# Performance work log

Hardware: AMD Instinct MI355X
Metric: run time of the kernel (lower is better)

The kernel has to match this reference:

```python
import jax, jax.numpy as jnp
import numpy as np

B, T, J, D_IN = 16, 128, 75, 3
HID, OUT, E = 64, 256, 300


def setup_inputs() -> dict:
    key = jax.random.key(0)
    ks = jax.random.split(key, 6)
    x = jax.random.normal(ks[0], (B, T, J, D_IN), dtype=jnp.float32)
    edge_index = jax.random.randint(ks[1], (2, E), 0, J, dtype=jnp.int64)
    W1 = jax.random.normal(ks[2], (D_IN, HID), dtype=jnp.float32) * (1.0 / np.sqrt(D_IN))
    b1 = jax.random.normal(ks[3], (HID,), dtype=jnp.float32) * 0.02
    W2 = jax.random.normal(ks[4], (HID, OUT), dtype=jnp.float32) * (1.0 / np.sqrt(HID))
    b2 = jax.random.normal(ks[5], (OUT,), dtype=jnp.float32) * 0.02
    return {"x": x, "edge_index": edge_index, "W1": W1, "b1": b1, "W2": W2, "b2": b2}


def _gcn_norm(edge_index, num_nodes, dtype):
    # PyG gcn_norm: add self-loops, norm = deg^{-1/2}[src] * deg^{-1/2}[dst]
    loops = jnp.arange(num_nodes, dtype=edge_index.dtype)
    src = jnp.concatenate([edge_index[0], loops])
    dst = jnp.concatenate([edge_index[1], loops])
    deg = jnp.zeros((num_nodes,), dtype).at[dst].add(jnp.ones_like(dst, dtype))
    dis = jax.lax.rsqrt(deg)  # deg >= 1 due to self loops
    norm = dis[src] * dis[dst]  # (E+J,)
    return src, dst, norm


def _gcn_layer(h, W, b, src, dst, norm):
    # h: (BT, J, Din) -> (BT, J, Dout). Linear first, then normalized scatter-add.
    h = h @ W
    msgs = h[:, src, :] * norm[None, :, None]        # (BT, E+J, Dout)
    agg = jnp.zeros_like(h).at[:, dst, :].add(msgs)  # (BT, J, Dout)
    return agg + b


def reference(x, edge_index, W1, b1, W2, b2):
    Bx, Tx, Jx, Dx = x.shape
    h = x.reshape(Bx * Tx, Jx, Dx)
    src, dst, norm = _gcn_norm(edge_index, Jx, x.dtype)
    h = jax.nn.gelu(_gcn_layer(h, W1, b1, src, dst, norm), approximate=False)
    h = jax.nn.gelu(_gcn_layer(h, W2, b2, src, dst, norm), approximate=False)
    return h.reshape(Bx, Tx, Jx, -1)
```

## Files before the change

### kernel.cpp

```cpp
#include <hip/hip_runtime.h>
#include <hip/hip_bf16.h>
#include <math.h>

#define J 75
#define EDGES 300
#define MAXE (EDGES + J)
#define HID 64
#define OUTF 256
#define BT 2048
#define MROWS 80
#define CSP 152

typedef __attribute__((ext_vector_type(8))) short short8;
typedef __attribute__((ext_vector_type(4))) float f32x4;

__device__ __forceinline__ unsigned short f32_to_bf16_rn(float f) {
    unsigned u = __float_as_uint(f);
    unsigned r = u + 0x7FFFu + ((u >> 16) & 1u);
    return (unsigned short)(r >> 16);
}
__device__ __forceinline__ float bf16_to_f32(unsigned short h) {
    return __uint_as_float(((unsigned)h) << 16);
}

__device__ __forceinline__ float gelu_fast(float v) {
    float u = 0.70710678118654752f * v;
    float a = fabsf(u);
    float t = __builtin_amdgcn_rcpf(fmaf(0.3275911f, a, 1.0f));
    float p = t * fmaf(t, fmaf(t, fmaf(t, fmaf(t, 1.061405429f, -1.453152027f),
                                       1.421413741f), -0.284496736f), 0.254829592f);
    float e = __expf(-a * a);
    float erfa = fmaf(-p, e, 1.0f);
    float erfu = copysignf(erfa, u);
    return 0.5f * v * (1.0f + erfu);
}

__global__ void prep_kernel(const int* __restrict__ ei,
                            const float* __restrict__ W2,
                            int* __restrict__ csr_off,
                            unsigned short* __restrict__ csr_src,
                            float* __restrict__ csr_norm,
                            unsigned short* __restrict__ Whi,
                            unsigned short* __restrict__ Wlo) {
    __shared__ int   deg[J];
    __shared__ int   off[J + 1];
    __shared__ int   cur[J];
    __shared__ float dis[J];
    const int tid = threadIdx.x;

    if (blockIdx.x < 64) {
        int t = blockIdx.x * 256 + tid;
        int j    = t & 7;
        int lane = (t >> 3) & 63;
        int nt   = (t >> 9) & 15;
        int kc   = t >> 13;
        int k = kc * 32 + (lane >> 4) * 8 + j;
        int n = nt * 16 + (lane & 15);
        float w = W2[k * OUTF + n];
        unsigned short hi = f32_to_bf16_rn(w);
        float lo = w - bf16_to_f32(hi);
        Whi[t] = hi;
        Wlo[t] = f32_to_bf16_rn(lo);
        return;
    }

    if (tid < J) { deg[tid] = 1; cur[tid] = 0; }
    __syncthreads();
    for (int e = tid; e < EDGES; e += 256)
        atomicAdd(&deg[ei[EDGES + e]], 1);
    __syncthreads();
    if (tid == 0) {
        int s = 0;
        for (int j = 0; j < J; ++j) { off[j] = s; s += deg[j]; }
        off[J] = s;
    }
    if (tid < J) dis[tid] = rsqrtf((float)deg[tid]);
    __syncthreads();
    for (int e = tid; e < EDGES; e += 256) {
        int s = ei[e], d = ei[EDGES + e];
        int p = off[d] + atomicAdd(&cur[d], 1);
        csr_src[p]  = (unsigned short)s;
        csr_norm[p] = dis[s] * dis[d];
    }
    for (int j = tid; j < J; j += 256) {
        int p = off[j] + atomicAdd(&cur[j], 1);
        csr_src[p]  = (unsigned short)j;
        csr_norm[p] = dis[j] * dis[j];
    }
    __syncthreads();
    for (int j = tid; j <= J; j += 256) csr_off[j] = off[j];
}

__global__ void __launch_bounds__(256, 3) gcn_fused_kernel(
        const float* __restrict__ xg,
        const float* __restrict__ W1,
        const float* __restrict__ b1,
        const float* __restrict__ b2,
        const int*   __restrict__ csr_off,
        const unsigned short* __restrict__ csr_src,
        const float* __restrict__ csr_norm,
        const unsigned short* __restrict__ Whi,
        const unsigned short* __restrict__ Wlo,
        float* __restrict__ outg) {
    __shared__ float xs[J * 3];
    __shared__ float ax[J * 3];
    __shared__ float Bs[J * HID];
    __shared__ __align__(16) unsigned short Csp[MROWS * CSP];
    __shared__ float W1s[3 * HID];
    __shared__ float b1s[HID];
    __shared__ float b2s[OUTF];
    __shared__ int   offs[J + 1];
    __shared__ unsigned short srcs[MAXE];
    __shared__ float nrms[MAXE];

    const int tid  = threadIdx.x;
    const int bt   = blockIdx.x;
    const int wv   = tid >> 6;
    const int lane = tid & 63;
    const int quad = lane >> 4;
    const int l16  = lane & 15;

    if (tid < J + 1) offs[tid] = csr_off[tid];
    for (int i = tid; i < MAXE; i += 256) { srcs[i] = csr_src[i]; nrms[i] = csr_norm[i]; }
    if (tid < 3 * HID) W1s[tid] = W1[tid];
    if (tid < HID)     b1s[tid] = b1[tid];
    if (tid < OUTF)    b2s[tid] = b2[tid];
    for (int i = tid; i < J * 3; i += 256)
        xs[i] = xg[bt * (J * 3) + i];
    __syncthreads();

    for (int idx = tid; idx < J * 3; idx += 256) {
        int j = idx / 3, d = idx - j * 3;
        float s = 0.f;
        int p0 = offs[j], p1 = offs[j + 1];
        for (int p = p0; p < p1; ++p) s += nrms[p] * xs[srcs[p] * 3 + d];
        ax[idx] = s;
    }
    __syncthreads();

    for (int idx = tid; idx < J * HID; idx += 256) {
        int j = idx >> 6, f = idx & 63;
        float v = ax[j * 3 + 0] * W1s[0 * HID + f]
                + ax[j * 3 + 1] * W1s[1 * HID + f]
                + ax[j * 3 + 2] * W1s[2 * HID + f]
                + b1s[f];
        Bs[idx] = gelu_fast(v);
    }
    __syncthreads();

    for (int idx = tid; idx < J * HID; idx += 256) {
        int j = idx >> 6, f = idx & 63;
        float s = 0.f, s2 = 0.f;
        int p0 = offs[j], p1 = offs[j + 1];
        int p = p0;
        for (; p + 1 < p1; p += 2) {
            int a = srcs[p], b = srcs[p + 1];
            float na = nrms[p], nb = nrms[p + 1];
            s  += na * Bs[a * HID + f];
            s2 += nb * Bs[b * HID + f];
        }
        if (p < p1) s += nrms[p] * Bs[srcs[p] * HID + f];
        s += s2;
        unsigned short hi = f32_to_bf16_rn(s);
        unsigned short lo = f32_to_bf16_rn(s - bf16_to_f32(hi));
        Csp[j * CSP + f]      = hi;
        Csp[j * CSP + 64 + f] = lo;
    }
    for (int idx = tid; idx < (MROWS - J) * 128; idx += 256) {
        int j = J + (idx >> 7), c = idx & 127;
        Csp[j * CSP + c] = 0;
    }
    __syncthreads();

    f32x4 acc[5][4];
#pragma unroll
    for (int n4 = 0; n4 < 4; ++n4) {
        float bv = b2s[wv * 64 + n4 * 16 + l16];
#pragma unroll
        for (int mt = 0; mt < 5; ++mt)
            acc[mt][n4] = (f32x4){bv, bv, bv, bv};
    }

    const short8* Whi8 = (const short8*)Whi;
    const short8* Wlo8 = (const short8*)Wlo;
#pragma unroll
    for (int kc = 0; kc < 2; ++kc) {
        short8 bhi[4], blo[4];
#pragma unroll
        for (int n4 = 0; n4 < 4; ++n4) {
            int nt = wv * 4 + n4;
            int fi = (kc * 16 + nt) * 64 + lane;
            bhi[n4] = Whi8[fi];
            blo[n4] = Wlo8[fi];
        }
#pragma unroll
        for (int mt = 0; mt < 5; ++mt) {
            const unsigned short* ar = &Csp[(mt * 16 + l16) * CSP + kc * 32 + quad * 8];
            short8 ahi = *(const short8*)ar;
            short8 alo = *(const short8*)(ar + 64);
#pragma unroll
            for (int n4 = 0; n4 < 4; ++n4) {
                acc[mt][n4] = __builtin_amdgcn_mfma_f32_16x16x32_bf16(ahi, bhi[n4], acc[mt][n4], 0, 0, 0);
                acc[mt][n4] = __builtin_amdgcn_mfma_f32_16x16x32_bf16(ahi, blo[n4], acc[mt][n4], 0, 0, 0);
                acc[mt][n4] = __builtin_amdgcn_mfma_f32_16x16x32_bf16(alo, bhi[n4], acc[mt][n4], 0, 0, 0);
            }
        }
    }

    float* outb = outg + (size_t)bt * (J * OUTF);
#pragma unroll
    for (int mt = 0; mt < 5; ++mt) {
#pragma unroll
        for (int n4 = 0; n4 < 4; ++n4) {
            int o = wv * 64 + n4 * 16 + l16;
#pragma unroll
            for (int r = 0; r < 4; ++r) {
                int row = mt * 16 + quad * 4 + r;
                if (row < J)
                    outb[row * OUTF + o] = gelu_fast(acc[mt][n4][r]);
            }
        }
    }
}

extern "C" void kernel_launch(void* const* d_in, const int* in_sizes, int n_in,
                              void* d_out, int out_size, void* d_ws, size_t ws_size,
                              hipStream_t stream) {
    const float* x  = (const float*)d_in[0];
    const int*   ei = (const int*)d_in[1];
    const float* W1 = (const float*)d_in[2];
    const float* b1 = (const float*)d_in[3];
    const float* W2 = (const float*)d_in[4];
    const float* b2 = (const float*)d_in[5];
    float* out = (float*)d_out;

    char* ws = (char*)d_ws;
    int*            csr_off  = (int*)ws;
    unsigned short* csr_src  = (unsigned short*)(ws + 512);
    float*          csr_norm = (float*)(ws + 2048);
    unsigned short* Whi      = (unsigned short*)(ws + 4096);
    unsigned short* Wlo      = (unsigned short*)(ws + 4096 + 32768);

    prep_kernel<<<65, 256, 0, stream>>>(ei, W2, csr_off, csr_src, csr_norm, Whi, Wlo);
    gcn_fused_kernel<<<BT, 256, 0, stream>>>(x, W1, b1, b2,
                                             csr_off, csr_src, csr_norm,
                                             Whi, Wlo, out);
}
```

Measured before the change: 221.3 us.

## Aggregate layer-2 via dense adjacency MFMA, tanh GELU, and higher occupancy

Precomputes a dense normalized adjacency matrix split into bf16 hi/lo fragments and performs the layer-2 neighbour aggregation as an MFMA matmul instead of a CSR gather loop. The W2 GEMM is split into two passes over output tiles to halve accumulator registers, and the launch bound rises to 4 blocks per CU with smaller LDS use. GELU is replaced by the tanh approximation, which is cheaper but deviates from the exact erf GELU in the reference.

```diff
diff --git a/kernel.cpp b/kernel.cpp
--- a/kernel.cpp
+++ b/kernel.cpp
@@ -8,8 +8,9 @@
 #define HID 64
 #define OUTF 256
 #define BT 2048
-#define MROWS 80
-#define CSP 152
+#define BSPW 66
+#define BSPROWS 96
+#define CSTR2 72
 
 typedef __attribute__((ext_vector_type(8))) short short8;
 typedef __attribute__((ext_vector_type(4))) float f32x4;
@@ -22,17 +23,13 @@
 __device__ __forceinline__ float bf16_to_f32(unsigned short h) {
     return __uint_as_float(((unsigned)h) << 16);
 }
-
 __device__ __forceinline__ float gelu_fast(float v) {
-    float u = 0.70710678118654752f * v;
-    float a = fabsf(u);
-    float t = __builtin_amdgcn_rcpf(fmaf(0.3275911f, a, 1.0f));
-    float p = t * fmaf(t, fmaf(t, fmaf(t, fmaf(t, 1.061405429f, -1.453152027f),
-                                       1.421413741f), -0.284496736f), 0.254829592f);
-    float e = __expf(-a * a);
-    float erfa = fmaf(-p, e, 1.0f);
-    float erfu = copysignf(erfa, u);
-    return 0.5f * v * (1.0f + erfu);
+    float v2 = v * v;
+    float t  = fmaf(v2, 0.044715f, 1.0f);
+    float z  = 0.7978845608028654f * v * t;
+    float e  = __expf(2.0f * z);
+    float r  = __builtin_amdgcn_rcpf(e + 1.0f);
+    return v * (1.0f - r);
 }
 
 __global__ void prep_kernel(const int* __restrict__ ei,
@@ -41,11 +38,9 @@
                             unsigned short* __restrict__ csr_src,
                             float* __restrict__ csr_norm,
                             unsigned short* __restrict__ Whi,
-                            unsigned short* __restrict__ Wlo) {
-    __shared__ int   deg[J];
-    __shared__ int   off[J + 1];
-    __shared__ int   cur[J];
-    __shared__ float dis[J];
+                            unsigned short* __restrict__ Wlo,
+                            unsigned short* __restrict__ Ahi,
+                            unsigned short* __restrict__ Alo) {
     const int tid = threadIdx.x;
 
     if (blockIdx.x < 64) {
@@ -58,40 +53,75 @@
         int n = nt * 16 + (lane & 15);
         float w = W2[k * OUTF + n];
         unsigned short hi = f32_to_bf16_rn(w);
-        float lo = w - bf16_to_f32(hi);
         Whi[t] = hi;
-        Wlo[t] = f32_to_bf16_rn(lo);
+        Wlo[t] = f32_to_bf16_rn(w - bf16_to_f32(hi));
         return;
     }
 
-    if (tid < J) { deg[tid] = 1; cur[tid] = 0; }
-    __syncthreads();
-    for (int e = tid; e < EDGES; e += 256)
-        atomicAdd(&deg[ei[EDGES + e]], 1);
-    __syncthreads();
-    if (tid == 0) {
-        int s = 0;
-        for (int j = 0; j < J; ++j) { off[j] = s; s += deg[j]; }
-        off[J] = s;
-    }
-    if (tid < J) dis[tid] = rsqrtf((float)deg[tid]);
+    if (blockIdx.x == 64) {
+        __shared__ int   deg[J];
+        __shared__ int   off[J + 1];
+        __shared__ int   cur[J];
+        __shared__ float dis[J];
+        if (tid < J) { deg[tid] = 1; cur[tid] = 0; }
+        __syncthreads();
+        for (int e = tid; e < EDGES; e += 256) atomicAdd(&deg[ei[EDGES + e]], 1);
+        __syncthreads();
+        if (tid == 0) {
+            int s = 0;
+            for (int j = 0; j < J; ++j) { off[j] = s; s += deg[j]; }
+            off[J] = s;
+        }
+        if (tid < J) dis[tid] = rsqrtf((float)deg[tid]);
+        __syncthreads();
+        for (int e = tid; e < EDGES; e += 256) {
+            int s = ei[e], d = ei[EDGES + e];
+            int p = off[d] + atomicAdd(&cur[d], 1);
+            csr_src[p]  = (unsigned short)s;
+            csr_norm[p] = dis[s] * dis[d];
+        }
+        for (int j = tid; j < J; j += 256) {
+            int p = off[j] + atomicAdd(&cur[j], 1);
+            csr_src[p]  = (unsigned short)j;
+            csr_norm[p] = dis[j] * dis[j];
+        }
+        __syncthreads();
+        for (int j = tid; j <= J; j += 256) csr_off[j] = off[j];
+        return;
+    }
+
+    __shared__ float Ad[80 * 96];
+    __shared__ int   deg2[J];
+    __shared__ float dis2[J];
+    for (int i = tid; i < 80 * 96; i += 256) Ad[i] = 0.f;
+    if (tid < J) deg2[tid] = 1;
+    __syncthreads();
+    for (int e = tid; e < EDGES; e += 256) atomicAdd(&deg2[ei[EDGES + e]], 1);
+    __syncthreads();
+    if (tid < J) dis2[tid] = rsqrtf((float)deg2[tid]);
     __syncthreads();
     for (int e = tid; e < EDGES; e += 256) {
         int s = ei[e], d = ei[EDGES + e];
-        int p = off[d] + atomicAdd(&cur[d], 1);
-        csr_src[p]  = (unsigned short)s;
-        csr_norm[p] = dis[s] * dis[d];
-    }
-    for (int j = tid; j < J; j += 256) {
-        int p = off[j] + atomicAdd(&cur[j], 1);
-        csr_src[p]  = (unsigned short)j;
-        csr_norm[p] = dis[j] * dis[j];
-    }
-    __syncthreads();
-    for (int j = tid; j <= J; j += 256) csr_off[j] = off[j];
-}
-
-__global__ void __launch_bounds__(256, 3) gcn_fused_kernel(
+        atomicAdd(&Ad[d * 96 + s], dis2[s] * dis2[d]);
+    }
+    __syncthreads();
+    if (tid < J) Ad[tid * 96 + tid] += dis2[tid] * dis2[tid];
+    __syncthreads();
+    for (int t = tid; t < 15 * 512; t += 256) {
+        int jj   = t & 7;
+        int lane = (t >> 3) & 63;
+        int f    = t >> 9;
+        int mt = f / 3, kc = f - mt * 3;
+        int m = mt * 16 + (lane & 15);
+        int k = kc * 32 + (lane >> 4) * 8 + jj;
+        float v = Ad[m * 96 + k];
+        unsigned short hi = f32_to_bf16_rn(v);
+        Ahi[t] = hi;
+        Alo[t] = f32_to_bf16_rn(v - bf16_to_f32(hi));
+    }
+}
+
+__global__ void __launch_bounds__(256, 4) gcn_fused_kernel(
         const float* __restrict__ xg,
         const float* __restrict__ W1,
         const float* __restrict__ b1,
@@ -101,11 +131,12 @@
         const float* __restrict__ csr_norm,
         const unsigned short* __restrict__ Whi,
         const unsigned short* __restrict__ Wlo,
+        const unsigned short* __restrict__ Ahi,
+        const unsigned short* __restrict__ Alo,
         float* __restrict__ outg) {
+    __shared__ __align__(16) unsigned int Ubuf[BSPROWS * BSPW];
     __shared__ float xs[J * 3];
     __shared__ float ax[J * 3];
-    __shared__ float Bs[J * HID];
-    __shared__ __align__(16) unsigned short Csp[MROWS * CSP];
     __shared__ float W1s[3 * HID];
     __shared__ float b1s[HID];
     __shared__ float b2s[OUTF];
@@ -125,8 +156,7 @@
     if (tid < 3 * HID) W1s[tid] = W1[tid];
     if (tid < HID)     b1s[tid] = b1[tid];
     if (tid < OUTF)    b2s[tid] = b2[tid];
-    for (int i = tid; i < J * 3; i += 256)
-        xs[i] = xg[bt * (J * 3) + i];
+    for (int i = tid; i < J * 3; i += 256) xs[i] = xg[bt * (J * 3) + i];
     __syncthreads();
 
     for (int idx = tid; idx < J * 3; idx += 256) {
@@ -144,80 +174,108 @@
                 + ax[j * 3 + 1] * W1s[1 * HID + f]
                 + ax[j * 3 + 2] * W1s[2 * HID + f]
                 + b1s[f];
-        Bs[idx] = gelu_fast(v);
-    }
-    __syncthreads();
-
-    for (int idx = tid; idx < J * HID; idx += 256) {
-        int j = idx >> 6, f = idx & 63;
-        float s = 0.f, s2 = 0.f;
-        int p0 = offs[j], p1 = offs[j + 1];
-        int p = p0;
-        for (; p + 1 < p1; p += 2) {
-            int a = srcs[p], b = srcs[p + 1];
-            float na = nrms[p], nb = nrms[p + 1];
-            s  += na * Bs[a * HID + f];
-            s2 += nb * Bs[b * HID + f];
-        }
-        if (p < p1) s += nrms[p] * Bs[srcs[p] * HID + f];
-        s += s2;
-        unsigned short hi = f32_to_bf16_rn(s);
-        unsigned short lo = f32_to_bf16_rn(s - bf16_to_f32(hi));
-        Csp[j * CSP + f]      = hi;
-        Csp[j * CSP + 64 + f] = lo;
-    }
-    for (int idx = tid; idx < (MROWS - J) * 128; idx += 256) {
-        int j = J + (idx >> 7), c = idx & 127;
-        Csp[j * CSP + c] = 0;
-    }
-    __syncthreads();
-
-    f32x4 acc[5][4];
-#pragma unroll
-    for (int n4 = 0; n4 < 4; ++n4) {
-        float bv = b2s[wv * 64 + n4 * 16 + l16];
-#pragma unroll
-        for (int mt = 0; mt < 5; ++mt)
-            acc[mt][n4] = (f32x4){bv, bv, bv, bv};
-    }
+        float g = gelu_fast(v);
+        unsigned short hi = f32_to_bf16_rn(g);
+        unsigned short lo = f32_to_bf16_rn(g - bf16_to_f32(hi));
+        Ubuf[j * BSPW + f] = (unsigned)hi | ((unsigned)lo << 16);
+    }
+    for (int idx = tid; idx < (BSPROWS - J) * BSPW; idx += 256) {
+        int r = J + idx / BSPW, c = idx - (idx / BSPW) * BSPW;
+        Ubuf[r * BSPW + c] = 0u;
+    }
+    __syncthreads();
+
+    f32x4 cacc[5] = {};
+    const short8* Ahi8 = (const short8*)Ahi;
+    const short8* Alo8 = (const short8*)Alo;
+#pragma unroll
+    for (int kc = 0; kc < 3; ++kc) {
+        unsigned w[8];
+#pragma unroll
+        for (int jj = 0; jj < 8; ++jj)
+            w[jj] = Ubuf[(kc * 32 + quad * 8 + jj) * BSPW + wv * 16 + l16];
+        short8 bh, bl;
+#pragma unroll
+        for (int jj = 0; jj < 8; ++jj) {
+            bh[jj] = (short)(w[jj] & 0xFFFFu);
+            bl[jj] = (short)(w[jj] >> 16);
+        }
+#pragma unroll
+        for (int mt = 0; mt < 5; ++mt) {
+            short8 ah = Ahi8[(mt * 3 + kc) * 64 + lane];
+            short8 al = Alo8[(mt * 3 + kc) * 64 + lane];
+            cacc[mt] = __builtin_amdgcn_mfma_f32_16x16x32_bf16(ah, bh, cacc[mt], 0, 0, 0);
+            cacc[mt] = __builtin_amdgcn_mfma_f32_16x16x32_bf16(ah, bl, cacc[mt], 0, 0, 0);
+            cacc[mt] = __builtin_amdgcn_mfma_f32_16x16x32_bf16(al, bh, cacc[mt], 0, 0, 0);
+        }
+    }
+    __syncthreads();
+
+    unsigned short* CH = (unsigned short*)Ubuf;
+    unsigned short* CL = CH + 80 * CSTR2;
+#pragma unroll
+    for (int mt = 0; mt < 5; ++mt) {
+#pragma unroll
+        for (int r = 0; r < 4; ++r) {
+            int node = mt * 16 + quad * 4 + r;
+            int feat = wv * 16 + l16;
+            float v = cacc[mt][r];
+            unsigned short hi = f32_to_bf16_rn(v);
+            unsigned short lo = f32_to_bf16_rn(v - bf16_to_f32(hi));
+            CH[node * CSTR2 + feat] = hi;
+            CL[node * CSTR2 + feat] = lo;
+        }
+    }
+    __syncthreads();
 
     const short8* Whi8 = (const short8*)Whi;
     const short8* Wlo8 = (const short8*)Wlo;
-#pragma unroll
-    for (int kc = 0; kc < 2; ++kc) {
-        short8 bhi[4], blo[4];
-#pragma unroll
-        for (int n4 = 0; n4 < 4; ++n4) {
-            int nt = wv * 4 + n4;
-            int fi = (kc * 16 + nt) * 64 + lane;
-            bhi[n4] = Whi8[fi];
-            blo[n4] = Wlo8[fi];
+    float* outb = outg + (size_t)bt * (J * OUTF);
+
+#pragma unroll
+    for (int p = 0; p < 2; ++p) {
+        f32x4 acc[5][2];
+#pragma unroll
+        for (int q2 = 0; q2 < 2; ++q2) {
+            int nt2 = wv * 4 + p * 2 + q2;
+            float bv = b2s[nt2 * 16 + l16];
+#pragma unroll
+            for (int mt = 0; mt < 5; ++mt) acc[mt][q2] = (f32x4){bv, bv, bv, bv};
+        }
+#pragma unroll
+        for (int kc = 0; kc < 2; ++kc) {
+            short8 wh[2], wl[2];
+#pragma unroll
+            for (int q2 = 0; q2 < 2; ++q2) {
+                int nt2 = wv * 4 + p * 2 + q2;
+                int fi = (kc * 16 + nt2) * 64 + lane;
+                wh[q2] = Whi8[fi];
+                wl[q2] = Wlo8[fi];
+            }
+#pragma unroll
+            for (int mt = 0; mt < 5; ++mt) {
+                const unsigned short* ab = &CH[(mt * 16 + l16) * CSTR2 + kc * 32 + quad * 8];
+                short8 ah = *(const short8*)ab;
+                short8 al = *(const short8*)(ab + 80 * CSTR2);
+#pragma unroll
+                for (int q2 = 0; q2 < 2; ++q2) {
+                    acc[mt][q2] = __builtin_amdgcn_mfma_f32_16x16x32_bf16(ah, wh[q2], acc[mt][q2], 0, 0, 0);
+                    acc[mt][q2] = __builtin_amdgcn_mfma_f32_16x16x32_bf16(ah, wl[q2], acc[mt][q2], 0, 0, 0);
+                    acc[mt][q2] = __builtin_amdgcn_mfma_f32_16x16x32_bf16(al, wh[q2], acc[mt][q2], 0, 0, 0);
+                }
+            }
         }
 #pragma unroll
         for (int mt = 0; mt < 5; ++mt) {
-            const unsigned short* ar = &Csp[(mt * 16 + l16) * CSP + kc * 32 + quad * 8];
-            short8 ahi = *(const short8*)ar;
-            short8 alo = *(const short8*)(ar + 64);
-#pragma unroll
-            for (int n4 = 0; n4 < 4; ++n4) {
-                acc[mt][n4] = __builtin_amdgcn_mfma_f32_16x16x32_bf16(ahi, bhi[n4], acc[mt][n4], 0, 0, 0);
-                acc[mt][n4] = __builtin_amdgcn_mfma_f32_16x16x32_bf16(ahi, blo[n4], acc[mt][n4], 0, 0, 0);
-                acc[mt][n4] = __builtin_amdgcn_mfma_f32_16x16x32_bf16(alo, bhi[n4], acc[mt][n4], 0, 0, 0);
-            }
-        }
-    }
-
-    float* outb = outg + (size_t)bt * (J * OUTF);
-#pragma unroll
-    for (int mt = 0; mt < 5; ++mt) {
-#pragma unroll
-        for (int n4 = 0; n4 < 4; ++n4) {
-            int o = wv * 64 + n4 * 16 + l16;
-#pragma unroll
-            for (int r = 0; r < 4; ++r) {
-                int row = mt * 16 + quad * 4 + r;
-                if (row < J)
-                    outb[row * OUTF + o] = gelu_fast(acc[mt][n4][r]);
+#pragma unroll
+            for (int q2 = 0; q2 < 2; ++q2) {
+                int o = (wv * 4 + p * 2 + q2) * 16 + l16;
+#pragma unroll
+                for (int r = 0; r < 4; ++r) {
+                    int row = mt * 16 + quad * 4 + r;
+                    if (row < J)
+                        outb[row * OUTF + o] = gelu_fast(acc[mt][q2][r]);
+                }
             }
         }
     }
@@ -239,10 +297,13 @@
     unsigned short* csr_src  = (unsigned short*)(ws + 512);
     float*          csr_norm = (float*)(ws + 2048);
     unsigned short* Whi      = (unsigned short*)(ws + 4096);
-    unsigned short* Wlo      = (unsigned short*)(ws + 4096 + 32768);
-
-    prep_kernel<<<65, 256, 0, stream>>>(ei, W2, csr_off, csr_src, csr_norm, Whi, Wlo);
+    unsigned short* Wlo      = (unsigned short*)(ws + 36864);
+    unsigned short* Ahi      = (unsigned short*)(ws + 69632);
+    unsigned short* Alo      = (unsigned short*)(ws + 86016);
+
+    prep_kernel<<<66, 256, 0, stream>>>(ei, W2, csr_off, csr_src, csr_norm,
+                                        Whi, Wlo, Ahi, Alo);
     gcn_fused_kernel<<<BT, 256, 0, stream>>>(x, W1, b1, b2,
                                              csr_off, csr_src, csr_norm,
-                                             Whi, Wlo, out);
-}
+                                             Whi, Wlo, Ahi, Alo, out);
+}
```

After: 209.6 us. 5.3% less time.
